# Kernel optimization log

Measured on AMD Instinct MI355X. Metric: run time of the kernel, lower is better.

The kernel has to match this reference:

```python
import jax, jax.numpy as jnp
import numpy as np

N, E = 50000, 800000
IN = HID = OUT = 128
H, L, EDIM = 4, 3, 3
C = HID // H  # per-head channels = 32
EPS = 1e-5
NEG_SLOPE = 0.2


def setup_inputs() -> dict:
    key = jax.random.key(0)
    ks = jax.random.split(key, 10)

    def p(k, shape, fan_in):
        return jax.random.normal(k, shape, jnp.float32) * (fan_in ** -0.5)

    return {
        "x": jax.random.normal(ks[0], (N, IN), jnp.float32),
        "edge_index": jax.random.randint(ks[1], (2, E), 0, N),
        "edge_attr": jax.random.normal(ks[2], (E, EDIM), jnp.float32),
        # stacked per-layer GATv2 params (layer0 in==hidden so shapes match)
        "Wl": p(ks[3], (L, HID, H * C), HID),   # lin_l (source)
        "Wr": p(ks[4], (L, HID, H * C), HID),   # lin_r (target)
        "We": p(ks[5], (L, EDIM, H * C), EDIM), # lin_edge
        "att": p(ks[6], (L, H, C), C),          # attention vector a
        "ln_w": jnp.ones((L, HID), jnp.float32),
        "ln_b": jnp.zeros((L, HID), jnp.float32),
        "Wout": p(ks[7], (HID, OUT), HID),      # final jk Linear
        "bout": jnp.zeros((OUT,), jnp.float32),
    }


def _gatv2_layer(h, src, dst, edge_attr, Wl, Wr, We, att):
    # h: [N, F]; returns [N, H*C]
    xl = (h @ Wl).reshape(N, H, C)            # source transform
    xr = (h @ Wr).reshape(N, H, C)            # target transform
    ea = (edge_attr @ We).reshape(E, H, C)
    m = xl[src] + xr[dst] + ea                # [E, H, C]
    m = jax.nn.leaky_relu(m, NEG_SLOPE)
    logits = jnp.einsum('ehc,hc->eh', m, att)  # [E, H]
    # segment softmax over incoming edges of each destination node
    lmax = jax.ops.segment_max(logits, dst, num_segments=N)  # [N, H]
    lmax = jnp.where(jnp.isfinite(lmax), lmax, 0.0)
    ex = jnp.exp(logits - lmax[dst])
    denom = jax.ops.segment_sum(ex, dst, num_segments=N)
    alpha = ex / (denom[dst] + 1e-16)          # [E, H]
    msg = xl[src] * alpha[:, :, None]          # [E, H, C]
    out = jax.ops.segment_sum(msg, dst, num_segments=N)
    return out.reshape(N, H * C)


def _graph_layernorm(h, w, b):
    # PyG LayerNorm(mode='graph'): normalize over ALL nodes and features of the graph
    mean = jnp.mean(h)
    var = jnp.mean((h - mean) ** 2)
    return (h - mean) * jax.lax.rsqrt(var + EPS) * w + b


def reference(x, edge_index, edge_attr, Wl, Wr, We, att, ln_w, ln_b, Wout, bout):
    src, dst = edge_index[0], edge_index[1]
    h = x
    for l in range(L):  # small fixed layer loop
        h = _gatv2_layer(h, src, dst, edge_attr, Wl[l], Wr[l], We[l], att[l])
        h = _graph_layernorm(h, ln_w[l], ln_b[l])
        h = jax.nn.gelu(h, approximate=False)
        # dropout = 0.0 -> identity
    return h @ Wout + bout
```

## Files before the change

kernel.cpp:

```cpp
#include <hip/hip_runtime.h>
#include <hip/hip_bf16.h>
#include <math.h>

#define HID 128
#define NHEAD 4
#define CH 32
#define NLAYER 3
#define EDIM 3
#define EPSLN 1e-5f
#define SLOPE 0.2f
#define RSLOTS 1024
#define PAD_W -1e30f
#define LOG2E 1.4426950408889634f

typedef __bf16 bf16x8 __attribute__((ext_vector_type(8)));
typedef float f32x4 __attribute__((ext_vector_type(4)));
typedef float f32x2 __attribute__((ext_vector_type(2)));

__device__ __forceinline__ float bflo(unsigned d) { return __uint_as_float(d << 16); }
__device__ __forceinline__ float bfhi(unsigned d) { return __uint_as_float(d & 0xffff0000u); }

#define DPP_ADD(x, ctrl) \
    (x + __int_as_float(__builtin_amdgcn_update_dpp(0, __float_as_int(x), ctrl, 0xf, 0xf, true)))

__global__ void k_count(const int* __restrict__ dst, int* __restrict__ deg, int E) {
    int i = blockIdx.x * blockDim.x + threadIdx.x;
    if (i < E) atomicAdd(&deg[dst[i]], 1);
}

__global__ __launch_bounds__(1024) void k_scan(const int* __restrict__ deg,
                                               int* __restrict__ outs,
                                               int N, int G) {
    __shared__ int sw[16];
    __shared__ int scarry;
    int tid = threadIdx.x, lane = tid & 63, wid = tid >> 6;
    if (tid == 0) scarry = 0;
    __syncthreads();
    for (int base = 0; base < G; base += 1024) {
        int i = base + tid;
        int v = 0;
        if (i < G) {
            int n0 = 4 * i;
            if (n0 + 3 < N) {
                int4 d4 = *(const int4*)&deg[n0];
                v = ((d4.x + 3) & ~3) + ((d4.y + 3) & ~3) +
                    ((d4.z + 3) & ~3) + ((d4.w + 3) & ~3);
            } else {
#pragma unroll
                for (int j = 0; j < 4; j++) {
                    int n = n0 + j;
                    if (n < N) v += (deg[n] + 3) & ~3;
                }
            }
        }
        int x = v;
#pragma unroll
        for (int o = 1; o < 64; o <<= 1) { int y = __shfl_up(x, o, 64); if (lane >= o) x += y; }
        if (lane == 63) sw[wid] = x;
        __syncthreads();
        int carry = scarry;
        if (tid < 16) {
            int s = sw[tid];
#pragma unroll
            for (int o = 1; o < 16; o <<= 1) { int y = __shfl_up(s, o, 64); if (tid >= o) s += y; }
            sw[tid] = s;
        }
        __syncthreads();
        int wofs = (wid == 0) ? 0 : sw[wid - 1];
        int incl = carry + wofs + x;
        if (i < G) outs[i] = incl - v;
        __syncthreads();
        if (tid == 0) scarry = carry + sw[15];
        __syncthreads();
    }
    if (tid == 0) outs[G] = scarry;
}

__global__ void k_nodepad(const int* __restrict__ deg, const int* __restrict__ groupstart,
                          int* __restrict__ slotbase, int* __restrict__ cursor,
                          int4* __restrict__ slots, int N) {
    int i = blockIdx.x * blockDim.x + threadIdx.x;
    if (i >= N) return;
    int g = i >> 2;
    int base = groupstart[g];
    int i0 = g * 4;
#pragma unroll
    for (int j = 0; j < 3; j++)
        if (i0 + j < i) base += (deg[i0 + j] + 3) & ~3;
    slotbase[i] = base;
    cursor[i] = base;
    int d = deg[i];
    int pd = (d + 3) & ~3;
    for (int j = d; j < pd; j++) slots[base + j] = make_int4(-1, 0, 0, 0);
}

__global__ void k_fill2(const int* __restrict__ src, const int* __restrict__ dst,
                        const float* __restrict__ eattr, int* __restrict__ cursor,
                        int4* __restrict__ slots, int E) {
    int i = blockIdx.x * blockDim.x + threadIdx.x;
    if (i < E) {
        int n = dst[i];
        int slot = atomicAdd(&cursor[n], 1);
        slots[slot] = make_int4(src[i], __float_as_int(eattr[3 * i]),
                                __float_as_int(eattr[3 * i + 1]),
                                __float_as_int(eattr[3 * i + 2]));
    }
}

__global__ __launch_bounds__(256) void k_wprep(const float* __restrict__ Wl,
                                               const float* __restrict__ Wr,
                                               const float* __restrict__ Wout,
                                               __hip_bfloat16* __restrict__ wz) {
    int b = blockIdx.x;
    const float* src = (b < 6) ? ((b & 1) ? Wr + (size_t)(b >> 1) * 16384
                                          : Wl + (size_t)(b >> 1) * 16384)
                               : Wout;
    for (int t = threadIdx.x; t < 16384; t += 256) {
        int j = t & 7, q = (t >> 3) & 63, n = (t >> 9) & 7, s = t >> 12;
        int k = s * 32 + (q >> 4) * 8 + j;
        int c = n * 16 + (q & 15);
        wz[(size_t)b * 16384 + t] = __float2bfloat16(src[k * 128 + c]);
    }
}

__global__ __launch_bounds__(256) void k_cast(const float* __restrict__ in,
                                              __hip_bfloat16* __restrict__ out, int n) {
    int i = (blockIdx.x * 256 + threadIdx.x) * 4;
    if (i < n) {
        float4 v = *(const float4*)&in[i];
        __hip_bfloat16 o[4] = {__float2bfloat16(v.x), __float2bfloat16(v.y),
                               __float2bfloat16(v.z), __float2bfloat16(v.w)};
        *(ushort4*)&out[i] = *(ushort4*)o;
    }
}

template <bool BF16OUT>
__global__ __launch_bounds__(256) void k_gemm_mfma(const __hip_bfloat16* __restrict__ Xb,
                                                   const __hip_bfloat16* __restrict__ Wz0,
                                                   const __hip_bfloat16* __restrict__ Wz1,
                                                   void* __restrict__ Y0v,
                                                   void* __restrict__ Y1v,
                                                   const float* __restrict__ bias, int N) {
    __shared__ __hip_bfloat16 sW[16384];
    const __hip_bfloat16* Wz = blockIdx.y ? Wz1 : Wz0;
    void* Yv = blockIdx.y ? Y1v : Y0v;
    int tid = threadIdx.x;
    {
        const float4* s4 = (const float4*)Wz;
        float4* d4 = (float4*)sW;
#pragma unroll
        for (int i = 0; i < 8; i++) d4[tid + 256 * i] = s4[tid + 256 * i];
    }
    __syncthreads();

    int wv = tid >> 6, lane = tid & 63;
    int quad = lane >> 4, l16 = lane & 15;
    int mbase = blockIdx.x * 128 + wv * 32;

    f32x4 acc[2][8];
#pragma unroll
    for (int mt = 0; mt < 2; mt++)
#pragma unroll
        for (int n = 0; n < 8; n++) acc[mt][n] = (f32x4){0.f, 0.f, 0.f, 0.f};

#pragma unroll
    for (int s = 0; s < 4; s++) {
        bf16x8 a[2];
#pragma unroll
        for (int mt = 0; mt < 2; mt++) {
            int row = mbase + mt * 16 + l16;
            row = (row < N) ? row : (N - 1);
            a[mt] = *(const bf16x8*)&Xb[(size_t)row * HID + s * 32 + quad * 8];
        }
#pragma unroll
        for (int n = 0; n < 8; n++) {
            bf16x8 b = *(const bf16x8*)&sW[((s * 8 + n) * 64 + lane) * 8];
            acc[0][n] = __builtin_amdgcn_mfma_f32_16x16x32_bf16(a[0], b, acc[0][n], 0, 0, 0);
            acc[1][n] = __builtin_amdgcn_mfma_f32_16x16x32_bf16(a[1], b, acc[1][n], 0, 0, 0);
        }
    }

    float bv[8];
#pragma unroll
    for (int n = 0; n < 8; n++) bv[n] = bias ? bias[n * 16 + l16] : 0.f;

#pragma unroll
    for (int mt = 0; mt < 2; mt++)
#pragma unroll
        for (int reg = 0; reg < 4; reg++) {
            int row = mbase + mt * 16 + quad * 4 + reg;
            if (row < N) {
                if (BF16OUT) {
                    __hip_bfloat16* yp = (__hip_bfloat16*)Yv + (size_t)row * HID + l16;
#pragma unroll
                    for (int n = 0; n < 8; n++) yp[n * 16] = __float2bfloat16(acc[mt][n][reg]);
                } else {
                    float* yp = (float*)Yv + (size_t)row * HID + l16;
#pragma unroll
                    for (int n = 0; n < 8; n++) yp[n * 16] = acc[mt][n][reg] + bv[n];
                }
            }
        }
}

__global__ __launch_bounds__(256) void k_aggregate(const __hip_bfloat16* __restrict__ xlb,
                                                   const __hip_bfloat16* __restrict__ xrb,
                                                   const int4* __restrict__ slots,
                                                   const int* __restrict__ deg,
                                                   const int* __restrict__ slotbase,
                                                   const float* __restrict__ We,
                                                   const float* __restrict__ att,
                                                   unsigned* __restrict__ tmpp,
                                                   float* __restrict__ red, int N) {
    int wid = threadIdx.x >> 6;
    int lane = threadIdx.x & 63;
    int node = blockIdx.x * 4 + wid;
    if (node >= N) return;
    int c0 = lane * 2;
    int head = lane >> 4;

    f32x2 we0, we1, we2;
    { float2 t = *(const float2*)&We[c0];            we0 = (f32x2){t.x, t.y}; }
    { float2 t = *(const float2*)&We[HID + c0];      we1 = (f32x2){t.x, t.y}; }
    { float2 t = *(const float2*)&We[2 * HID + c0];  we2 = (f32x2){t.x, t.y}; }
    float at0 = att[head * CH + (c0 & 31)] * LOG2E;
    float at1 = att[head * CH + (c0 & 31) + 1] * LOG2E;

    int base = __builtin_amdgcn_readfirstlane(slotbase[node]);
    int steps = __builtin_amdgcn_readfirstlane((deg[node] + 3) >> 2);

    unsigned dxr = *(const unsigned*)&xrb[(size_t)node * HID + c0];
    f32x2 xr2 = (f32x2){bflo(dxr), bfhi(dxr)};

    float l = 0.f;
    f32x2 Av = (f32x2){0.f, 0.f};

    const int4* vp = slots + base;

#define GATH2(v, d) { int si = max((v).x, 0); \
    d = *(const unsigned*)&xlb[(size_t)si * HID + c0]; }

#define EDGE(v, d) {                                                          \
    float e0 = __int_as_float((v).y);                                         \
    float e1 = __int_as_float((v).z);                                         \
    float e2 = __int_as_float((v).w);                                         \
    float padw = ((v).x < 0) ? PAD_W : 0.f;                                   \
    f32x2 xv = (f32x2){bflo(d), bfhi(d)};                                     \
    f32x2 m = __builtin_elementwise_fma(we2, (f32x2)e2, xv + xr2);            \
    m = __builtin_elementwise_fma(we1, (f32x2)e1, m);                         \
    m = __builtin_elementwise_fma(we0, (f32x2)e0, m);                         \
    m = __builtin_elementwise_max(m, m * SLOPE);                              \
    float part = fmaf(m.x, at0, m.y * at1);                                   \
    part = DPP_ADD(part, 0xB1);                      \
    part = DPP_ADD(part, 0x4E);                      \
    part = DPP_ADD(part, 0x141);                    \
    part = DPP_ADD(part, 0x140);                        \
    float p = __builtin_amdgcn_exp2f(part + padw);                            \
    l += p;                                                                   \
    Av = __builtin_elementwise_fma((f32x2)p, xv, Av);                         \
}

    int t = 0;
    for (; t + 2 <= steps; t += 2) {
        int4 v0 = vp[4 * t + 0], v1 = vp[4 * t + 1], v2 = vp[4 * t + 2], v3 = vp[4 * t + 3];
        int4 v4 = vp[4 * t + 4], v5 = vp[4 * t + 5], v6 = vp[4 * t + 6], v7 = vp[4 * t + 7];
        unsigned d0, d1, d2, d3, d4, d5, d6, d7;
        GATH2(v0, d0); GATH2(v1, d1); GATH2(v2, d2); GATH2(v3, d3);
        GATH2(v4, d4); GATH2(v5, d5); GATH2(v6, d6); GATH2(v7, d7);
        EDGE(v0, d0); EDGE(v1, d1); EDGE(v2, d2); EDGE(v3, d3);
        EDGE(v4, d4); EDGE(v5, d5); EDGE(v6, d6); EDGE(v7, d7);
    }
    if (t < steps) {
        int4 v0 = vp[4 * t + 0], v1 = vp[4 * t + 1], v2 = vp[4 * t + 2], v3 = vp[4 * t + 3];
        unsigned d0, d1, d2, d3;
        GATH2(v0, d0); GATH2(v1, d1); GATH2(v2, d2); GATH2(v3, d3);
        EDGE(v0, d0); EDGE(v1, d1); EDGE(v2, d2); EDGE(v3, d3);
    }
#undef GATH2
#undef EDGE

    float inv = 1.f / (l + 1e-16f);
    f32x2 o2 = Av * inv;
    __hip_bfloat16 pk[2] = {__float2bfloat16(o2.x), __float2bfloat16(o2.y)};
    tmpp[(size_t)node * (HID / 2) + lane] = *(unsigned*)pk;

    float ssum = o2.x + o2.y;
    float ssq = fmaf(o2.x, o2.x, o2.y * o2.y);
#pragma unroll
    for (int o = 32; o >= 1; o >>= 1) { ssum += __shfl_xor(ssum, o); ssq += __shfl_xor(ssq, o); }
    if (lane == 0) {
        int slot = (node & (RSLOTS - 1)) * 2;
        atomicAdd(&red[slot], ssum);
        atomicAdd(&red[slot + 1], ssq);
    }
}

__global__ __launch_bounds__(256) void k_ln_gelu(const uint4* __restrict__ in4,
                                                 const float* __restrict__ w,
                                                 const float* __restrict__ b,
                                                 const float* __restrict__ red,
                                                 float M,
                                                 uint4* __restrict__ out4, int n8) {
    __shared__ float ls[8];
    int tid = threadIdx.x;
    float s = 0.f, q = 0.f;
    const float2* r2 = (const float2*)red;
    for (int i = tid; i < RSLOTS; i += 256) { float2 rv = r2[i]; s += rv.x; q += rv.y; }
#pragma unroll
    for (int o = 32; o >= 1; o >>= 1) { s += __shfl_xor(s, o); q += __shfl_xor(q, o); }
    if ((tid & 63) == 0) { ls[(tid >> 6) * 2] = s; ls[(tid >> 6) * 2 + 1] = q; }
    __syncthreads();
    float S = ls[0] + ls[2] + ls[4] + ls[6];
    float Q = ls[1] + ls[3] + ls[5] + ls[7];
    float mean = S / M;
    float inv = rsqrtf(Q / M - mean * mean + EPSLN);

    int i = blockIdx.x * blockDim.x + tid;
    if (i >= n8) return;
    uint4 v = in4[i];
    int col = (i * 8) & 127;
    float4 w0 = *(const float4*)&w[col], w1 = *(const float4*)&w[col + 4];
    float4 b0 = *(const float4*)&b[col], b1 = *(const float4*)&b[col + 4];
    float r[8] = {bflo(v.x), bfhi(v.x), bflo(v.y), bfhi(v.y),
                  bflo(v.z), bfhi(v.z), bflo(v.w), bfhi(v.w)};
    float wr[8] = {w0.x, w0.y, w0.z, w0.w, w1.x, w1.y, w1.z, w1.w};
    float br[8] = {b0.x, b0.y, b0.z, b0.w, b1.x, b1.y, b1.z, b1.w};
    __hip_bfloat16 o[8];
#pragma unroll
    for (int j = 0; j < 8; j++) {
        float t = fmaf((r[j] - mean) * inv, wr[j], br[j]);
        o[j] = __float2bfloat16(0.5f * t * (1.f + erff(t * 0.70710678118654752f)));
    }
    out4[i] = *(uint4*)o;
}

extern "C" void kernel_launch(void* const* d_in, const int* in_sizes, int n_in,
                              void* d_out, int out_size, void* d_ws, size_t ws_size,
                              hipStream_t stream) {
    const float* x = (const float*)d_in[0];
    const int* ei = (const int*)d_in[1];
    const float* eattr = (const float*)d_in[2];
    const float* Wl = (const float*)d_in[3];
    const float* Wr = (const float*)d_in[4];
    const float* We = (const float*)d_in[5];
    const float* att = (const float*)d_in[6];
    const float* lnw = (const float*)d_in[7];
    const float* lnb = (const float*)d_in[8];
    const float* Wout = (const float*)d_in[9];
    const float* bout = (const float*)d_in[10];
    float* out = (float*)d_out;

    int N = in_sizes[0] / HID;
    int E = in_sizes[1] / 2;
    int G = (N + 3) / 4;
    int SCAP = E + 8 * N;
    const int* src = ei;
    const int* dst = ei + E;

    char* w = (char*)d_ws;
    __hip_bfloat16* hb = (__hip_bfloat16*)w;   w += (size_t)N * HID * 2;
    __hip_bfloat16* xlb = (__hip_bfloat16*)w;  w += (size_t)N * HID * 2;
    __hip_bfloat16* xrb = (__hip_bfloat16*)w;  w += (size_t)N * HID * 2;
    unsigned* tmpp = (unsigned*)w;             w += (size_t)N * HID * 2;
    __hip_bfloat16* wz = (__hip_bfloat16*)w;   w += (size_t)7 * 16384 * 2;
    int4* slots = (int4*)w;       w += (size_t)SCAP * 16;
    int* deg = (int*)w;           w += (size_t)N * 4;
    int* cursor = (int*)w;        w += (size_t)N * 4;
    float* red = (float*)w;       w += (size_t)NLAYER * RSLOTS * 2 * 4;
    int* slotbase = (int*)w;      w += (size_t)N * 4;
    int* groupstart = (int*)w;    w += (size_t)(G + 1) * 4;

    hipMemsetAsync(deg, 0, (size_t)(2 * N + NLAYER * RSLOTS * 2) * 4, stream);
    k_count<<<(E + 255) / 256, 256, 0, stream>>>(dst, deg, E);
    k_scan<<<1, 1024, 0, stream>>>(deg, groupstart, N, G);
    k_nodepad<<<(N + 255) / 256, 256, 0, stream>>>(deg, groupstart, slotbase, cursor, slots, N);
    k_fill2<<<(E + 255) / 256, 256, 0, stream>>>(src, dst, eattr, cursor, slots, E);
    k_wprep<<<7, 256, 0, stream>>>(Wl, Wr, Wout, wz);
    k_cast<<<(N * HID / 4 + 255) / 256, 256, 0, stream>>>(x, hb, N * HID);

    int gb = (N + 127) / 128;
    float M = (float)N * (float)HID;
    for (int l = 0; l < NLAYER; l++) {
        float* redl = red + (size_t)l * RSLOTS * 2;
        k_gemm_mfma<true><<<dim3(gb, 2), 256, 0, stream>>>(
            hb, wz + (size_t)(2 * l) * 16384, wz + (size_t)(2 * l + 1) * 16384,
            xlb, xrb, nullptr, N);
        k_aggregate<<<(N + 3) / 4, 256, 0, stream>>>(
            xlb, xrb, slots, deg, slotbase,
            We + (size_t)l * EDIM * HID, att + (size_t)l * NHEAD * CH, tmpp, redl, N);
        k_ln_gelu<<<((N * HID / 8) + 255) / 256, 256, 0, stream>>>(
            (const uint4*)tmpp, lnw + (size_t)l * HID, lnb + (size_t)l * HID, redl, M,
            (uint4*)hb, N * HID / 8);
    }
    k_gemm_mfma<false><<<dim3(gb, 1), 256, 0, stream>>>(
        hb, wz + (size_t)6 * 16384, wz + (size_t)6 * 16384, out, out, bout, N);
}
```

Before: 430.7 us.

## Fuse LayerNorm+GELU and input cast into GEMM A-operand load

Removes the standalone k_ln_gelu and k_cast kernels. The GEMM now loads either fp32 x and converts it to bf16, or loads the pre-norm bf16 aggregate, reduces the layer statistics per block, and applies LayerNorm and GELU in registers before the MFMA. This drops one full N×128 write and read per layer plus several launches. In exchange, the erf-based GELU is recomputed redundantly: the dual-output GEMM (grid y=2) computes it twice per element, and each block repeats the 1024-slot statistics reduction.

```diff
diff --git a/kernel.cpp b/kernel.cpp
--- a/kernel.cpp
+++ b/kernel.cpp
@@ -123,25 +123,20 @@
     }
 }
 
-__global__ __launch_bounds__(256) void k_cast(const float* __restrict__ in,
-                                              __hip_bfloat16* __restrict__ out, int n) {
-    int i = (blockIdx.x * 256 + threadIdx.x) * 4;
-    if (i < n) {
-        float4 v = *(const float4*)&in[i];
-        __hip_bfloat16 o[4] = {__float2bfloat16(v.x), __float2bfloat16(v.y),
-                               __float2bfloat16(v.z), __float2bfloat16(v.w)};
-        *(ushort4*)&out[i] = *(ushort4*)o;
-    }
-}
-
-template <bool BF16OUT>
-__global__ __launch_bounds__(256) void k_gemm_mfma(const __hip_bfloat16* __restrict__ Xb,
+template <int AIN, bool BF16OUT>
+__global__ __launch_bounds__(256) void k_gemm_mfma(const void* __restrict__ Xv,
                                                    const __hip_bfloat16* __restrict__ Wz0,
                                                    const __hip_bfloat16* __restrict__ Wz1,
                                                    void* __restrict__ Y0v,
                                                    void* __restrict__ Y1v,
-                                                   const float* __restrict__ bias, int N) {
+                                                   const float* __restrict__ bias,
+                                                   const float* __restrict__ lnw,
+                                                   const float* __restrict__ lnb,
+                                                   const float* __restrict__ red,
+                                                   float M, int N) {
     __shared__ __hip_bfloat16 sW[16384];
+    __shared__ float swb[256];
+    __shared__ float ls[8];
     const __hip_bfloat16* Wz = blockIdx.y ? Wz1 : Wz0;
     void* Yv = blockIdx.y ? Y1v : Y0v;
     int tid = threadIdx.x;
@@ -151,7 +146,24 @@
 #pragma unroll
         for (int i = 0; i < 8; i++) d4[tid + 256 * i] = s4[tid + 256 * i];
     }
+    if (AIN == 1) {
+        if (tid < 128) swb[tid] = lnw[tid];
+        else swb[tid] = lnb[tid - 128];
+        float s = 0.f, q = 0.f;
+        const float2* r2 = (const float2*)red;
+        for (int i = tid; i < RSLOTS; i += 256) { float2 rv = r2[i]; s += rv.x; q += rv.y; }
+#pragma unroll
+        for (int o = 32; o >= 1; o >>= 1) { s += __shfl_xor(s, o); q += __shfl_xor(q, o); }
+        if ((tid & 63) == 0) { ls[(tid >> 6) * 2] = s; ls[(tid >> 6) * 2 + 1] = q; }
+    }
     __syncthreads();
+    float mean = 0.f, inv = 0.f;
+    if (AIN == 1) {
+        float S = ls[0] + ls[2] + ls[4] + ls[6];
+        float Q = ls[1] + ls[3] + ls[5] + ls[7];
+        mean = S / M;
+        inv = rsqrtf(Q / M - mean * mean + EPSLN);
+    }
 
     int wv = tid >> 6, lane = tid & 63;
     int quad = lane >> 4, l16 = lane & 15;
@@ -170,7 +182,33 @@
         for (int mt = 0; mt < 2; mt++) {
             int row = mbase + mt * 16 + l16;
             row = (row < N) ? row : (N - 1);
-            a[mt] = *(const bf16x8*)&Xb[(size_t)row * HID + s * 32 + quad * 8];
+            int chb = s * 32 + quad * 8;
+            if (AIN == 0) {
+                const float* X = (const float*)Xv;
+                float4 u0 = *(const float4*)&X[(size_t)row * HID + chb];
+                float4 u1 = *(const float4*)&X[(size_t)row * HID + chb + 4];
+                __hip_bfloat16 h[8] = {__float2bfloat16(u0.x), __float2bfloat16(u0.y),
+                                       __float2bfloat16(u0.z), __float2bfloat16(u0.w),
+                                       __float2bfloat16(u1.x), __float2bfloat16(u1.y),
+                                       __float2bfloat16(u1.z), __float2bfloat16(u1.w)};
+                a[mt] = *(bf16x8*)h;
+            } else {
+                const unsigned* T = (const unsigned*)Xv;
+                uint4 v = *(const uint4*)&T[(size_t)row * (HID / 2) + (chb >> 1)];
+                float4 w0 = *(const float4*)&swb[chb], w1 = *(const float4*)&swb[chb + 4];
+                float4 b0 = *(const float4*)&swb[128 + chb], b1 = *(const float4*)&swb[128 + chb + 4];
+                float r[8] = {bflo(v.x), bfhi(v.x), bflo(v.y), bfhi(v.y),
+                              bflo(v.z), bfhi(v.z), bflo(v.w), bfhi(v.w)};
+                float wr[8] = {w0.x, w0.y, w0.z, w0.w, w1.x, w1.y, w1.z, w1.w};
+                float br[8] = {b0.x, b0.y, b0.z, b0.w, b1.x, b1.y, b1.z, b1.w};
+                __hip_bfloat16 h[8];
+#pragma unroll
+                for (int j = 0; j < 8; j++) {
+                    float t = fmaf((r[j] - mean) * inv, wr[j], br[j]);
+                    h[j] = __float2bfloat16(0.5f * t * (1.f + erff(t * 0.70710678118654752f)));
+                }
+                a[mt] = *(bf16x8*)h;
+            }
         }
 #pragma unroll
         for (int n = 0; n < 8; n++) {
@@ -295,45 +333,6 @@
     }
 }
 
-__global__ __launch_bounds__(256) void k_ln_gelu(const uint4* __restrict__ in4,
-                                                 const float* __restrict__ w,
-                                                 const float* __restrict__ b,
-                                                 const float* __restrict__ red,
-                                                 float M,
-                                                 uint4* __restrict__ out4, int n8) {
-    __shared__ float ls[8];
-    int tid = threadIdx.x;
-    float s = 0.f, q = 0.f;
-    const float2* r2 = (const float2*)red;
-    for (int i = tid; i < RSLOTS; i += 256) { float2 rv = r2[i]; s += rv.x; q += rv.y; }
-#pragma unroll
-    for (int o = 32; o >= 1; o >>= 1) { s += __shfl_xor(s, o); q += __shfl_xor(q, o); }
-    if ((tid & 63) == 0) { ls[(tid >> 6) * 2] = s; ls[(tid >> 6) * 2 + 1] = q; }
-    __syncthreads();
-    float S = ls[0] + ls[2] + ls[4] + ls[6];
-    float Q = ls[1] + ls[3] + ls[5] + ls[7];
-    float mean = S / M;
-    float inv = rsqrtf(Q / M - mean * mean + EPSLN);
-
-    int i = blockIdx.x * blockDim.x + tid;
-    if (i >= n8) return;
-    uint4 v = in4[i];
-    int col = (i * 8) & 127;
-    float4 w0 = *(const float4*)&w[col], w1 = *(const float4*)&w[col + 4];
-    float4 b0 = *(const float4*)&b[col], b1 = *(const float4*)&b[col + 4];
-    float r[8] = {bflo(v.x), bfhi(v.x), bflo(v.y), bfhi(v.y),
-                  bflo(v.z), bfhi(v.z), bflo(v.w), bfhi(v.w)};
-    float wr[8] = {w0.x, w0.y, w0.z, w0.w, w1.x, w1.y, w1.z, w1.w};
-    float br[8] = {b0.x, b0.y, b0.z, b0.w, b1.x, b1.y, b1.z, b1.w};
-    __hip_bfloat16 o[8];
-#pragma unroll
-    for (int j = 0; j < 8; j++) {
-        float t = fmaf((r[j] - mean) * inv, wr[j], br[j]);
-        o[j] = __float2bfloat16(0.5f * t * (1.f + erff(t * 0.70710678118654752f)));
-    }
-    out4[i] = *(uint4*)o;
-}
-
 extern "C" void kernel_launch(void* const* d_in, const int* in_sizes, int n_in,
                               void* d_out, int out_size, void* d_ws, size_t ws_size,
                               hipStream_t stream) {
@@ -358,7 +357,6 @@
     const int* dst = ei + E;
 
     char* w = (char*)d_ws;
-    __hip_bfloat16* hb = (__hip_bfloat16*)w;   w += (size_t)N * HID * 2;
     __hip_bfloat16* xlb = (__hip_bfloat16*)w;  w += (size_t)N * HID * 2;
     __hip_bfloat16* xrb = (__hip_bfloat16*)w;  w += (size_t)N * HID * 2;
     unsigned* tmpp = (unsigned*)w;             w += (size_t)N * HID * 2;
@@ -376,22 +374,27 @@
     k_nodepad<<<(N + 255) / 256, 256, 0, stream>>>(deg, groupstart, slotbase, cursor, slots, N);
     k_fill2<<<(E + 255) / 256, 256, 0, stream>>>(src, dst, eattr, cursor, slots, E);
     k_wprep<<<7, 256, 0, stream>>>(Wl, Wr, Wout, wz);
-    k_cast<<<(N * HID / 4 + 255) / 256, 256, 0, stream>>>(x, hb, N * HID);
 
     int gb = (N + 127) / 128;
     float M = (float)N * (float)HID;
     for (int l = 0; l < NLAYER; l++) {
         float* redl = red + (size_t)l * RSLOTS * 2;
-        k_gemm_mfma<true><<<dim3(gb, 2), 256, 0, stream>>>(
-            hb, wz + (size_t)(2 * l) * 16384, wz + (size_t)(2 * l + 1) * 16384,
-            xlb, xrb, nullptr, N);
+        if (l == 0) {
+            k_gemm_mfma<0, true><<<dim3(gb, 2), 256, 0, stream>>>(
+                x, wz, wz + 16384, xlb, xrb, nullptr, nullptr, nullptr, nullptr, 0.f, N);
+        } else {
+            k_gemm_mfma<1, true><<<dim3(gb, 2), 256, 0, stream>>>(
+                tmpp, wz + (size_t)(2 * l) * 16384, wz + (size_t)(2 * l + 1) * 16384,
+                xlb, xrb, nullptr,
+                lnw + (size_t)(l - 1) * HID, lnb + (size_t)(l - 1) * HID,
+                red + (size_t)(l - 1) * RSLOTS * 2, M, N);
+        }
         k_aggregate<<<(N + 3) / 4, 256, 0, stream>>>(
             xlb, xrb, slots, deg, slotbase,
             We + (size_t)l * EDIM * HID, att + (size_t)l * NHEAD * CH, tmpp, redl, N);
-        k_ln_gelu<<<((N * HID / 8) + 255) / 256, 256, 0, stream>>>(
-            (const uint4*)tmpp, lnw + (size_t)l * HID, lnb + (size_t)l * HID, redl, M,
-            (uint4*)hb, N * HID / 8);
-    }
-    k_gemm_mfma<false><<<dim3(gb, 1), 256, 0, stream>>>(
-        hb, wz + (size_t)6 * 16384, wz + (size_t)6 * 16384, out, out, bout, N);
-}
+    }
+    k_gemm_mfma<1, false><<<dim3(gb, 1), 256, 0, stream>>>(
+        tmpp, wz + (size_t)6 * 16384, wz + (size_t)6 * 16384, out, out, bout,
+        lnw + (size_t)2 * HID, lnb + (size_t)2 * HID,
+        red + (size_t)2 * RSLOTS * 2, M, N);
+}
```

Measured after the change: 433.7 us. Within noise of the previous version (+0.7%).
